# Performance work log

Measured on AMD Instinct MI355X. Metric: run time of the kernel, lower is better.

## Reference

```python
import jax, jax.numpy as jnp
import numpy as np

WORD = 512
ED = 64


def setup_inputs() -> dict:
    key = jax.random.key(0)
    ks = jax.random.split(key, 7)
    x = jax.random.normal(ks[0], (4, 4096, WORD), dtype=jnp.float32)
    # Dense layer params (kernel + bias) for query/key/value projections
    s = 1.0 / np.sqrt(WORD)
    Wq = jax.random.normal(ks[1], (WORD, ED), dtype=jnp.float32) * s
    Wk = jax.random.normal(ks[2], (WORD, ED), dtype=jnp.float32) * s
    Wv = jax.random.normal(ks[3], (WORD, ED), dtype=jnp.float32) * s
    bq = jnp.zeros((ED,), dtype=jnp.float32)
    bk = jnp.zeros((ED,), dtype=jnp.float32)
    bv = jnp.zeros((ED,), dtype=jnp.float32)
    return {"x": x, "Wq": Wq, "bq": bq, "Wk": Wk, "bk": bk, "Wv": Wv, "bv": bv}


def reference(x, Wq, bq, Wk, bk, Wv, bv):
    # Q, K, V: [B, S, ED]
    Q = jnp.einsum('bsw,we->bse', x, Wq) + bq
    K = jnp.einsum('bsw,we->bse', x, Wk) + bk
    V = jnp.einsum('bsw,we->bse', x, Wv) + bv
    scale = 1.0 / jnp.sqrt(jnp.float32(ED))
    score = jnp.einsum('bqe,bke->bqk', Q, K) * scale  # [B, S, S]
    attn = jax.nn.softmax(score, axis=-1)
    Z = jnp.einsum('bqk,bke->bqe', attn, V)  # [B, S, ED]
    return Z
```

## Files before the change

kernel.cpp:

```cpp
#include <hip/hip_runtime.h>
#include <cstdint>


typedef __bf16 bf16x8 __attribute__((ext_vector_type(8)));
typedef float f32x4 __attribute__((ext_vector_type(4)));
typedef float f32x16 __attribute__((ext_vector_type(16)));
typedef int i32x2 __attribute__((ext_vector_type(2)));

#define SCALEQ 0.18033688011112042f

#define WT_OFF 0u
#define Q_OFF  262144u
#define KV_OFF 2359296u
#define L_OFF  6553600u
#define OP_OFF 7077888u

#if defined(__has_builtin)
#if __has_builtin(__builtin_amdgcn_permlane32_swap)
#define HAVE_PLSWAP 1
#endif
#if __has_builtin(__builtin_amdgcn_global_load_lds)
#define HAVE_GLL 1
#endif
#endif
#ifndef HAVE_PLSWAP
#define HAVE_PLSWAP 0
#endif
#ifndef HAVE_GLL
#define HAVE_GLL 0
#endif

__device__ __forceinline__ unsigned short bf16_1(float a) {
  unsigned ua = __builtin_bit_cast(unsigned, a);
  ua += 0x7FFFu + ((ua >> 16) & 1u);
  return (unsigned short)(ua >> 16);
}
__device__ __forceinline__ unsigned cvtpk(float lo, float hi) {
  unsigned r;
  asm("v_cvt_pk_bf16_f32 %0, %1, %2" : "=v"(r) : "v"(lo), "v"(hi));
  return r;
}
__device__ __forceinline__ void plswap(unsigned& x, unsigned& y, unsigned hl) {
#if HAVE_PLSWAP
  i32x2 r = __builtin_amdgcn_permlane32_swap((int)x, (int)y, false, false);
  x = (unsigned)r[0];
  y = (unsigned)r[1];
#else
  unsigned xs = (unsigned)__shfl_xor((int)x, 32);
  unsigned ys = (unsigned)__shfl_xor((int)y, 32);
  unsigned nx = hl ? ys : x;
  unsigned ny = hl ? y : xs;
  x = nx;
  y = ny;
#endif
}
#if HAVE_GLL
__device__ __forceinline__ void gll16(const void* g, void* l) {
  __builtin_amdgcn_global_load_lds(
      (const __attribute__((address_space(1))) void*)g,
      (__attribute__((address_space(3))) void*)l, 16, 0, 0);
}
#endif

__global__ __launch_bounds__(256) void prep_w(const float* __restrict__ Wq,
                                              const float* __restrict__ Wk,
                                              const float* __restrict__ Wv,
                                              unsigned short* __restrict__ wt2) {
  unsigned gtid = blockIdx.x * 256u + threadIdx.x;
  unsigned mat = gtid >> 15, rem = gtid & 32767u;
  const float* w = (mat == 0) ? Wq : (mat == 1) ? Wk : Wv;
  float v = w[rem];
  unsigned k = rem >> 6, n = rem & 63u;
  unsigned col = mat * 64u + n;
  unsigned ntg = col >> 4, l15c = col & 15u;
  unsigned kc = k >> 5, quad = (k >> 3) & 3u, j = k & 7u;
  wt2[((ntg * 16u + kc) * 64u + quad * 16u + l15c) * 8u + j] = bf16_1(v);
}

__global__ __launch_bounds__(256, 4) void qkv_proj(
    const float* __restrict__ x, const unsigned short* __restrict__ wt2,
    const float* __restrict__ bq, const float* __restrict__ bk,
    const float* __restrict__ bv, unsigned short* __restrict__ qws,
    unsigned short* __restrict__ kvws) {
  __shared__ __align__(16) char xs[32768];
  __shared__ float biasl[192];
  const unsigned t = threadIdx.x;
  const unsigned row0 = blockIdx.x * 32u;
  const unsigned w = t >> 6, lane = t & 63u, l15 = lane & 15u, quad = lane >> 4;

  if (t < 192u) {
    unsigned mat = t >> 6, n = t & 63u;
    biasl[t] = (mat == 0) ? bq[n] : (mat == 1) ? bk[n] : bv[n];
  }
#pragma unroll
  for (int i = 0; i < 16; i++) {
    unsigned idx4 = t + 256u * (unsigned)i;
    unsigned fidx = idx4 * 4u;
    unsigned row = fidx >> 9, k = fidx & 511u, g = k >> 3;
    float4 f = *(const float4*)(x + row0 * 512u + fidx);
    int2 v = make_int2((int)cvtpk(f.x, f.y), (int)cvtpk(f.z, f.w));
    *(int2*)(xs + row * 1024u + ((g ^ (row & 7u)) << 4) + (k & 7u) * 2u) = v;
  }
  __syncthreads();

  f32x4 acc[2][3];
#pragma unroll
  for (int rg = 0; rg < 2; rg++)
#pragma unroll
    for (int i = 0; i < 3; i++) acc[rg][i] = {0.f, 0.f, 0.f, 0.f};
  const unsigned short* wbase = wt2 + (w * 3u * 1024u + lane) * 8u;

  int4 cur[3], nxt[3];
#pragma unroll
  for (int nt = 0; nt < 3; nt++)
    cur[nt] = *(const int4*)(wbase + (unsigned)nt * 8192u);
  for (unsigned kc = 0; kc < 16u; kc++) {
    if (kc < 15u) {
#pragma unroll
      for (int nt = 0; nt < 3; nt++)
        nxt[nt] = *(const int4*)(wbase + ((unsigned)nt * 16u + kc + 1u) * 512u);
    }
    unsigned ag = kc * 4u + quad;
    unsigned r1 = 16u + l15;
    int4 av0 = *(const int4*)(xs + l15 * 1024u + ((ag ^ (l15 & 7u)) << 4));
    int4 av1 = *(const int4*)(xs + r1 * 1024u + ((ag ^ (r1 & 7u)) << 4));
    bf16x8 a0 = __builtin_bit_cast(bf16x8, av0);
    bf16x8 a1 = __builtin_bit_cast(bf16x8, av1);
#pragma unroll
    for (int nt = 0; nt < 3; nt++)
      acc[0][nt] = __builtin_amdgcn_mfma_f32_16x16x32_bf16(
          a0, __builtin_bit_cast(bf16x8, cur[nt]), acc[0][nt], 0, 0, 0);
#pragma unroll
    for (int nt = 0; nt < 3; nt++)
      acc[1][nt] = __builtin_amdgcn_mfma_f32_16x16x32_bf16(
          a1, __builtin_bit_cast(bf16x8, cur[nt]), acc[1][nt], 0, 0, 0);
#pragma unroll
    for (int nt = 0; nt < 3; nt++) cur[nt] = nxt[nt];
  }
#pragma unroll
  for (int rg = 0; rg < 2; rg++) {
    unsigned sb = row0 + (unsigned)rg * 16u + quad * 4u;
#pragma unroll
    for (int nt = 0; nt < 3; nt++) {
      unsigned col = w * 48u + (unsigned)nt * 16u + l15;
      unsigned mat = col >> 6, n = col & 63u;
      float bb = biasl[col];
      if (mat == 0) {
#pragma unroll
        for (int r = 0; r < 4; r++)
          qws[(sb + (unsigned)r) * 64u + n] =
              bf16_1((acc[rg][nt][r] + bb) * SCALEQ);
      } else if (mat == 1) {
#pragma unroll
        for (int r = 0; r < 4; r++) {
          unsigned s = sb + (unsigned)r;
          unsigned bb2 = s >> 12, tile = (s & 4095u) >> 6, kap = s & 63u;
          kvws[(bb2 * 64u + tile) * 8192u + (n >> 3) * 512u + kap * 8u +
               (n & 7u)] = bf16_1(acc[rg][nt][r] + bb);
        }
      } else {
        unsigned s = sb;
        unsigned bb2 = s >> 12, tile = (s & 4095u) >> 6;
        unsigned kg = (s & 63u) >> 3, j0 = s & 7u;
        int2 pv =
            make_int2((int)cvtpk(acc[rg][nt][0] + bb, acc[rg][nt][1] + bb),
                      (int)cvtpk(acc[rg][nt][2] + bb, acc[rg][nt][3] + bb));
        *(int2*)(kvws + (bb2 * 64u + tile) * 8192u + (8u + kg) * 512u + n * 8u +
                 j0) = pv;
      }
    }
  }
}

__global__ __launch_bounds__(256, 2) void attn(
    const unsigned short* __restrict__ qws,
    const unsigned short* __restrict__ kvws, float* __restrict__ lws,
    unsigned short* __restrict__ opp) {
  __shared__ __align__(16) char sm[34816];
  const unsigned t = threadIdx.x;
  const unsigned w = t >> 6, lane = t & 63u, l31 = lane & 31u, hl = lane >> 5;
  const unsigned bid = blockIdx.x;
  const unsigned ks = bid >> 6;
  const unsigned qb = bid & 63u;
  const unsigned b = qb >> 4;
  const unsigned s0 = (qb & 15u) * 256u + w * 64u;
  const unsigned short* kvb = kvws + (b * 64u + ks * 8u) * 8192u + lane * 8u;

  bf16x8 qf[2][4];
#pragma unroll
  for (int qt2 = 0; qt2 < 2; qt2++)
#pragma unroll
    for (int kq = 0; kq < 4; kq++)
      qf[qt2][kq] = __builtin_bit_cast(
          bf16x8,
          *(const int4*)(qws + (b * 4096u + s0 + (unsigned)qt2 * 32u + l31) * 64u +
                         (unsigned)kq * 16u + hl * 8u));
  f32x16 accO[2][2];
#pragma unroll
  for (int qt2 = 0; qt2 < 2; qt2++)
#pragma unroll
    for (int dh = 0; dh < 2; dh++)
#pragma unroll
      for (int r = 0; r < 16; r++) accO[qt2][dh][r] = 0.f;
  float lsumA = 0.f, lsumB = 0.f;

#if HAVE_GLL
#define STAGE(kt_, bi_)                                                \
  {                                                                    \
    _Pragma("unroll") for (int i = 0; i < 4; i++) {                    \
      unsigned c = (unsigned)i * 4u + w;                               \
      gll16(kvb + (kt_)*8192u + c * 512u, sm + (bi_)*16384u + c * 1024u); \
    }                                                                  \
  }
  STAGE(0u, 0u);
  __syncthreads();
#else
  int4 stg[4];
#define LOADT(kt_)                                                         \
  {                                                                        \
    _Pragma("unroll") for (int i = 0; i < 4; i++) stg[i] =                 \
        *(const int4*)(kvb + (kt_)*8192u + ((unsigned)i * 4u + w) * 512u); \
  }
  LOADT(0u);
  {
#pragma unroll
    for (int i = 0; i < 4; i++)
      *(int4*)(sm + ((unsigned)i * 4u + w) * 1024u + lane * 16u) = stg[i];
  }
  __syncthreads();
#endif

#pragma unroll 1
  for (unsigned kt = 0; kt < 8u; kt++) {
    char* kb = sm + (kt & 1u) * 16384u;
    int4 kfr[8], vfr[8];
#pragma unroll
    for (int kq = 0; kq < 4; kq++)
#pragma unroll
      for (int kh = 0; kh < 2; kh++)
        kfr[kq * 2 + kh] = *(const int4*)(
            kb + (((unsigned)kq * 2u + hl) * 64u + (unsigned)kh * 32u + l31) * 16u);
#pragma unroll
    for (int kqg = 0; kqg < 4; kqg++)
#pragma unroll
      for (int dh = 0; dh < 2; dh++)
        vfr[kqg * 2 + dh] = *(const int4*)(
            kb + 8192u +
            (((unsigned)kqg * 2u + hl) * 64u + (unsigned)dh * 32u + l31) * 16u);
#if HAVE_GLL
    if (kt < 7u) STAGE(kt + 1u, (kt + 1u) & 1u);
#else
    if (kt < 7u) LOADT(kt + 1u);
#endif
    __builtin_amdgcn_s_setprio(1);
#pragma unroll
    for (int kh = 0; kh < 2; kh++) {
      f32x16 zA, zB;
#pragma unroll
      for (int r = 0; r < 16; r++) zA[r] = 0.f;
#pragma unroll
      for (int r = 0; r < 16; r++) zB[r] = 0.f;
#pragma unroll
      for (int kq = 0; kq < 4; kq++)
        zA = __builtin_amdgcn_mfma_f32_32x32x16_bf16(
            __builtin_bit_cast(bf16x8, kfr[kq * 2 + kh]), qf[0][kq], zA, 0, 0, 0);
#pragma unroll
      for (int kq = 0; kq < 4; kq++)
        zB = __builtin_amdgcn_mfma_f32_32x32x16_bf16(
            __builtin_bit_cast(bf16x8, kfr[kq * 2 + kh]), qf[1][kq], zB, 0, 0, 0);
#pragma unroll
      for (int r = 0; r < 16; r++) zA[r] = __builtin_amdgcn_exp2f(zA[r]);
#pragma unroll
      for (int r = 0; r < 16; r++) zB[r] = __builtin_amdgcn_exp2f(zB[r]);
      {
        float s0a = (zA[0] + zA[1]) + (zA[2] + zA[3]);
        float s1a = (zA[4] + zA[5]) + (zA[6] + zA[7]);
        float s2a = (zA[8] + zA[9]) + (zA[10] + zA[11]);
        float s3a = (zA[12] + zA[13]) + (zA[14] + zA[15]);
        lsumA += (s0a + s1a) + (s2a + s3a);
        float s0b = (zB[0] + zB[1]) + (zB[2] + zB[3]);
        float s1b = (zB[4] + zB[5]) + (zB[6] + zB[7]);
        float s2b = (zB[8] + zB[9]) + (zB[10] + zB[11]);
        float s3b = (zB[12] + zB[13]) + (zB[14] + zB[15]);
        lsumB += (s0b + s1b) + (s2b + s3b);
      }
      unsigned pkA[8], pkB[8];
#pragma unroll
      for (int c2 = 0; c2 < 4; c2++) {
        pkA[2 * c2] = cvtpk(zA[4 * c2 + 0], zA[4 * c2 + 1]);
        pkA[2 * c2 + 1] = cvtpk(zA[4 * c2 + 2], zA[4 * c2 + 3]);
        pkB[2 * c2] = cvtpk(zB[4 * c2 + 0], zB[4 * c2 + 1]);
        pkB[2 * c2 + 1] = cvtpk(zB[4 * c2 + 2], zB[4 * c2 + 3]);
      }
#pragma unroll
      for (int kqpl = 0; kqpl < 2; kqpl++) {
        unsigned kqg = (unsigned)kh * 2u + (unsigned)kqpl;
        unsigned a0 = pkA[4 * kqpl + 0], a1 = pkA[4 * kqpl + 1];
        unsigned b0 = pkA[4 * kqpl + 2], b1 = pkA[4 * kqpl + 3];
        plswap(a0, b0, hl);
        plswap(a1, b1, hl);
        int4 frA = make_int4((int)a0, (int)a1, (int)b0, (int)b1);
        bf16x8 pfA = __builtin_bit_cast(bf16x8, frA);
#pragma unroll
        for (int dh = 0; dh < 2; dh++)
          accO[0][dh] = __builtin_amdgcn_mfma_f32_32x32x16_bf16(
              __builtin_bit_cast(bf16x8, vfr[kqg * 2u + (unsigned)dh]), pfA,
              accO[0][dh], 0, 0, 0);
        unsigned c0 = pkB[4 * kqpl + 0], c1 = pkB[4 * kqpl + 1];
        unsigned d0 = pkB[4 * kqpl + 2], d1 = pkB[4 * kqpl + 3];
        plswap(c0, d0, hl);
        plswap(c1, d1, hl);
        int4 frB = make_int4((int)c0, (int)c1, (int)d0, (int)d1);
        bf16x8 pfB = __builtin_bit_cast(bf16x8, frB);
#pragma unroll
        for (int dh = 0; dh < 2; dh++)
          accO[1][dh] = __builtin_amdgcn_mfma_f32_32x32x16_bf16(
              __builtin_bit_cast(bf16x8, vfr[kqg * 2u + (unsigned)dh]), pfB,
              accO[1][dh], 0, 0, 0);
      }
    }
    __builtin_amdgcn_s_setprio(0);
    __syncthreads();
#if !HAVE_GLL
    if (kt < 7u) {
#pragma unroll
      for (int i = 0; i < 4; i++)
        *(int4*)(sm + ((kt + 1u) & 1u) * 16384u +
                 ((unsigned)i * 4u + w) * 1024u + lane * 16u) = stg[i];
      __syncthreads();
    }
#endif
  }
  float* sc = (float*)(sm + w * 8704u);
#pragma unroll
  for (int qt2 = 0; qt2 < 2; qt2++) {
    float ls = (qt2 == 0) ? lsumA : lsumB;
    float lt = ls + __shfl_xor(ls, 32);
    unsigned qrow = s0 + (unsigned)qt2 * 32u;
    if (hl == 0u) lws[ks * 16384u + b * 4096u + qrow + l31] = lt;
#pragma unroll
    for (int dh = 0; dh < 2; dh++)
#pragma unroll
      for (int r = 0; r < 16; r++) {
        unsigned d = (unsigned)dh * 32u + (unsigned)(r & 3) +
                     8u * (unsigned)(r >> 2) + 4u * hl;
        sc[l31 * 68u + d] = accO[qt2][dh][r];
      }
#pragma unroll
    for (int i = 0; i < 4; i++) {
      unsigned ql = (lane >> 3) + (unsigned)i * 8u;
      unsigned d0 = (lane & 7u) * 8u;
      float4 f0 = *(const float4*)(sc + ql * 68u + d0);
      float4 f1 = *(const float4*)(sc + ql * 68u + d0 + 4u);
      int4 pv = make_int4((int)cvtpk(f0.x, f0.y), (int)cvtpk(f0.z, f0.w),
                          (int)cvtpk(f1.x, f1.y), (int)cvtpk(f1.z, f1.w));
      *(int4*)(opp + ks * 1048576u + (b * 4096u + qrow + ql) * 64u + d0) = pv;
    }
  }
}

__global__ __launch_bounds__(256) void combine(const unsigned short* __restrict__ opp,
                                               const float* __restrict__ lws,
                                               float* __restrict__ out) {
#pragma unroll
  for (int ii = 0; ii < 2; ii++) {
    unsigned slot = blockIdx.x * 512u + threadIdx.x + 256u * (unsigned)ii;
    unsigned q = slot >> 4, c = (slot & 15u) * 4u;
    float l = 0.f;
#pragma unroll
    for (int s = 0; s < 8; s++) l += lws[(unsigned)s * 16384u + q];
    float inv = 1.0f / l;
    float4 r = make_float4(0.f, 0.f, 0.f, 0.f);
#pragma unroll
    for (int s = 0; s < 8; s++) {
      int2 pv = *(const int2*)(opp + (unsigned)s * 1048576u + q * 64u + c);
      r.x += __builtin_bit_cast(float, (unsigned)pv.x << 16);
      r.y += __builtin_bit_cast(float, (unsigned)pv.x & 0xFFFF0000u);
      r.z += __builtin_bit_cast(float, (unsigned)pv.y << 16);
      r.w += __builtin_bit_cast(float, (unsigned)pv.y & 0xFFFF0000u);
    }
    r.x *= inv; r.y *= inv; r.z *= inv; r.w *= inv;
    *(float4*)(out + q * 64u + c) = r;
  }
}

extern "C" void kernel_launch(void* const* d_in, const int* in_sizes, int n_in,
                              void* d_out, int out_size, void* d_ws,
                              size_t ws_size, hipStream_t stream) {
  const float* x = (const float*)d_in[0];
  const float* Wq = (const float*)d_in[1];
  const float* bq = (const float*)d_in[2];
  const float* Wk = (const float*)d_in[3];
  const float* bk = (const float*)d_in[4];
  const float* Wv = (const float*)d_in[5];
  const float* bv = (const float*)d_in[6];
  char* ws = (char*)d_ws;
  unsigned short* wt2 = (unsigned short*)(ws + WT_OFF);
  unsigned short* qb = (unsigned short*)(ws + Q_OFF);
  unsigned short* kvb = (unsigned short*)(ws + KV_OFF);
  float* lp = (float*)(ws + L_OFF);
  unsigned short* opp = (unsigned short*)(ws + OP_OFF);
  float* outp = (float*)d_out;

  prep_w<<<384, 256, 0, stream>>>(Wq, Wk, Wv, wt2);
  qkv_proj<<<512, 256, 0, stream>>>(x, wt2, bq, bk, bv, qb, kvb);
  attn<<<512, 256, 0, stream>>>(qb, kvb, lp, opp);
  combine<<<512, 256, 0, stream>>>(opp, lp, outp);
}
```

Measured before the change: 115.7 us.

## Fuse split-KV combine into attention via last-block atomic counter

Removes the separate combine kernel launch. Each attention block now increments a per-query-block atomic counter after writing its partial outputs, and the last of the 8 KV-split blocks reduces the partials and writes the final output. The counters are zeroed in prep_w. This saves one launch and its tail, but adds a threadfence and atomic per block and serializes the reduction onto the last-arriving block of each group.

```diff
diff --git a/kernel.cpp b/kernel.cpp
--- a/kernel.cpp
+++ b/kernel.cpp
@@ -14,6 +14,7 @@
 #define KV_OFF 2359296u
 #define L_OFF  6553600u
 #define OP_OFF 7077888u
+#define CTR_OFF 23855104u
 
 #if defined(__has_builtin)
 #if __has_builtin(__builtin_amdgcn_permlane32_swap)
@@ -65,8 +66,10 @@
 __global__ __launch_bounds__(256) void prep_w(const float* __restrict__ Wq,
                                               const float* __restrict__ Wk,
                                               const float* __restrict__ Wv,
-                                              unsigned short* __restrict__ wt2) {
+                                              unsigned short* __restrict__ wt2,
+                                              unsigned* __restrict__ ctr) {
   unsigned gtid = blockIdx.x * 256u + threadIdx.x;
+  if (gtid < 64u) ctr[gtid] = 0u;
   unsigned mat = gtid >> 15, rem = gtid & 32767u;
   const float* w = (mat == 0) ? Wq : (mat == 1) ? Wk : Wv;
   float v = w[rem];
@@ -175,8 +178,10 @@
 __global__ __launch_bounds__(256, 2) void attn(
     const unsigned short* __restrict__ qws,
     const unsigned short* __restrict__ kvws, float* __restrict__ lws,
-    unsigned short* __restrict__ opp) {
+    unsigned short* __restrict__ opp, unsigned* __restrict__ ctr,
+    float* __restrict__ out) {
   __shared__ __align__(16) char sm[34816];
+  __shared__ unsigned sdone;
   const unsigned t = threadIdx.x;
   const unsigned w = t >> 6, lane = t & 63u, l31 = lane & 31u, hl = lane >> 5;
   const unsigned bid = blockIdx.x;
@@ -357,30 +362,42 @@
       *(int4*)(opp + ks * 1048576u + (b * 4096u + qrow + ql) * 64u + d0) = pv;
     }
   }
-}
-
-__global__ __launch_bounds__(256) void combine(const unsigned short* __restrict__ opp,
-                                               const float* __restrict__ lws,
-                                               float* __restrict__ out) {
-#pragma unroll
-  for (int ii = 0; ii < 2; ii++) {
-    unsigned slot = blockIdx.x * 512u + threadIdx.x + 256u * (unsigned)ii;
-    unsigned q = slot >> 4, c = (slot & 15u) * 4u;
-    float l = 0.f;
-#pragma unroll
-    for (int s = 0; s < 8; s++) l += lws[(unsigned)s * 16384u + q];
-    float inv = 1.0f / l;
-    float4 r = make_float4(0.f, 0.f, 0.f, 0.f);
-#pragma unroll
-    for (int s = 0; s < 8; s++) {
-      int2 pv = *(const int2*)(opp + (unsigned)s * 1048576u + q * 64u + c);
-      r.x += __builtin_bit_cast(float, (unsigned)pv.x << 16);
-      r.y += __builtin_bit_cast(float, (unsigned)pv.x & 0xFFFF0000u);
-      r.z += __builtin_bit_cast(float, (unsigned)pv.y << 16);
-      r.w += __builtin_bit_cast(float, (unsigned)pv.y & 0xFFFF0000u);
-    }
-    r.x *= inv; r.y *= inv; r.z *= inv; r.w *= inv;
-    *(float4*)(out + q * 64u + c) = r;
+  __threadfence();
+  __syncthreads();
+  if (t == 0u) sdone = atomicAdd(&ctr[qb], 1u);
+  __syncthreads();
+  if (sdone == 7u) {
+    __threadfence();
+    unsigned qbase = b * 4096u + (qb & 15u) * 256u;
+#pragma unroll 1
+    for (int i = 0; i < 8; i++) {
+      unsigned slot = (unsigned)i * 256u + t;
+      unsigned qo = slot >> 3, c = (slot & 7u) * 8u;
+      unsigned q = qbase + qo;
+      float l = 0.f;
+#pragma unroll
+      for (int s2 = 0; s2 < 8; s2++) l += lws[(unsigned)s2 * 16384u + q];
+      float inv = 1.0f / l;
+      float r[8];
+#pragma unroll
+      for (int j = 0; j < 8; j++) r[j] = 0.f;
+#pragma unroll
+      for (int s2 = 0; s2 < 8; s2++) {
+        int4 pv = *(const int4*)(opp + (unsigned)s2 * 1048576u + q * 64u + c);
+        r[0] += __builtin_bit_cast(float, (unsigned)pv.x << 16);
+        r[1] += __builtin_bit_cast(float, (unsigned)pv.x & 0xFFFF0000u);
+        r[2] += __builtin_bit_cast(float, (unsigned)pv.y << 16);
+        r[3] += __builtin_bit_cast(float, (unsigned)pv.y & 0xFFFF0000u);
+        r[4] += __builtin_bit_cast(float, (unsigned)pv.z << 16);
+        r[5] += __builtin_bit_cast(float, (unsigned)pv.z & 0xFFFF0000u);
+        r[6] += __builtin_bit_cast(float, (unsigned)pv.w << 16);
+        r[7] += __builtin_bit_cast(float, (unsigned)pv.w & 0xFFFF0000u);
+      }
+      float4 o0 = make_float4(r[0] * inv, r[1] * inv, r[2] * inv, r[3] * inv);
+      float4 o1 = make_float4(r[4] * inv, r[5] * inv, r[6] * inv, r[7] * inv);
+      *(float4*)(out + q * 64u + c) = o0;
+      *(float4*)(out + q * 64u + c + 4u) = o1;
+    }
   }
 }
 
@@ -400,10 +417,10 @@
   unsigned short* kvb = (unsigned short*)(ws + KV_OFF);
   float* lp = (float*)(ws + L_OFF);
   unsigned short* opp = (unsigned short*)(ws + OP_OFF);
+  unsigned* ctr = (unsigned*)(ws + CTR_OFF);
   float* outp = (float*)d_out;
 
-  prep_w<<<384, 256, 0, stream>>>(Wq, Wk, Wv, wt2);
+  prep_w<<<384, 256, 0, stream>>>(Wq, Wk, Wv, wt2, ctr);
   qkv_proj<<<512, 256, 0, stream>>>(x, wt2, bq, bk, bv, qb, kvb);
-  attn<<<512, 256, 0, stream>>>(qb, kvb, lp, opp);
-  combine<<<512, 256, 0, stream>>>(opp, lp, outp);
-}
+  attn<<<512, 256, 0, stream>>>(qb, kvb, lp, opp, ctr, outp);
+}
```

Result: slower. 178.9 us (+54.6%).
